# Kernel optimization log

Hardware: AMD Instinct MI355X
Metric: run time of the kernel (lower is better)

Reference implementation:

```python
import jax, jax.numpy as jnp
import numpy as np

E = 2048        # embed_dim
H = 16          # num_heads
HKV = 4         # num_heads_kv (GQA)
D = 128         # head_dim
DCONV = 4       # causal depthwise conv width
ROT_DIM = 128   # rotary_emb_dim (= head_dim, full rotation)
ROT_BASE = 10000.0
QKV_DIM = D * (H + 2 * HKV)  # 3072
B, S = 2, 2048


def setup_inputs() -> dict:
    key = jax.random.key(0)
    ks = jax.random.split(key, 7)
    return {
        "x": jax.random.normal(ks[0], (B, S, E), jnp.float32),
        "W_in": jax.random.normal(ks[1], (E, QKV_DIM), jnp.float32) * 0.02,
        "b_in": jax.random.normal(ks[2], (QKV_DIM,), jnp.float32) * 0.02,
        "conv_w": jax.random.normal(ks[3], (QKV_DIM, DCONV), jnp.float32) * 0.1,
        "conv_b": jax.random.normal(ks[4], (QKV_DIM,), jnp.float32) * 0.02,
        "W_out": jax.random.normal(ks[5], (E, E), jnp.float32) * 0.02,
        "b_out": jax.random.normal(ks[6], (E,), jnp.float32) * 0.02,
    }


def _rotary_cos_sin(seqlen, dtype):
    # flash_attn RotaryEmbedding: inv_freq over even indices
    inv_freq = 1.0 / (ROT_BASE ** (np.arange(0, ROT_DIM, 2, dtype=np.float32) / ROT_DIM))
    t = np.arange(seqlen, dtype=np.float32)
    freqs = np.outer(t, inv_freq)                      # [S, ROT_DIM/2]
    return jnp.asarray(np.cos(freqs), dtype), jnp.asarray(np.sin(freqs), dtype)


def _apply_rotary(xh, cos, sin):
    # non-interleaved: rotate halves of the first ROT_DIM dims. xh: [B,S,h,D]
    x1 = xh[..., : ROT_DIM // 2]
    x2 = xh[..., ROT_DIM // 2 : ROT_DIM]
    c = cos[None, :, None, :]
    s = sin[None, :, None, :]
    rot = jnp.concatenate([x1 * c - x2 * s, x2 * c + x1 * s], axis=-1)
    return jnp.concatenate([rot, xh[..., ROT_DIM:]], axis=-1)


def _forward(x, W_in, b_in, conv_w, conv_b, W_out, b_out):
    b, s, _ = x.shape
    qkv = x @ W_in + b_in                              # [B,S,QKV_DIM]

    # causal depthwise conv1d (kernel DCONV, left-pad DCONV-1, trim right)
    xp = jnp.pad(qkv, ((0, 0), (DCONV - 1, 0), (0, 0)))
    conv = conv_b
    for k in range(DCONV):
        conv = conv + xp[:, k : k + s, :] * conv_w[:, k]
    qkv = conv                                         # [B,S,QKV_DIM]

    q, kv = jnp.split(qkv, [H * D], axis=-1)
    q = q.reshape(b, s, H, D)
    kv = kv.reshape(b, s, 2, HKV, D)
    k, v = kv[:, :, 0], kv[:, :, 1]                    # [B,S,HKV,D]

    cos, sin = _rotary_cos_sin(s, x.dtype)
    q = _apply_rotary(q, cos, sin)
    k = _apply_rotary(k, cos, sin)

    # GQA: repeat kv heads
    rep = H // HKV
    k = jnp.repeat(k, rep, axis=2)                     # [B,S,H,D]
    v = jnp.repeat(v, rep, axis=2)

    scale = 1.0 / np.sqrt(D)
    scores = jnp.einsum("bqhd,bkhd->bhqk", q, k) * scale
    causal = jnp.tril(jnp.ones((s, s), bool))
    scores = jnp.where(causal[None, None], scores, jnp.finfo(scores.dtype).min)
    probs = jax.nn.softmax(scores, axis=-1)
    ctx = jnp.einsum("bhqk,bkhd->bqhd", probs, v)      # [B,S,H,D]

    return ctx.reshape(b, s, H * D) @ W_out + b_out    # [B,S,E]


def reference(x, W_in, b_in, conv_w, conv_b, W_out, b_out):
    return _forward(x, W_in, b_in, conv_w, conv_b, W_out, b_out)
```

## Files before the change

### kernel.cpp

```cpp
#include <hip/hip_runtime.h>
#include <hip/hip_bf16.h>

#define B_    2
#define S_    2048
#define E_    2048
#define H_    16
#define HKV_  4
#define D_    128
#define QKV_  3072

#define LOG2E  1.4426950408889634f
#define SCALE  0.08838834764831845f
#define SL     0.127517431f

typedef __attribute__((ext_vector_type(8))) short short8;
typedef __attribute__((ext_vector_type(4))) float floatx4;

typedef __attribute__((address_space(1))) const unsigned int gu32;
typedef __attribute__((address_space(3))) unsigned int lu32;

__device__ __forceinline__ void load_lds16(const unsigned short* g, unsigned short* l) {
    __builtin_amdgcn_global_load_lds((gu32*)g, (lu32*)l, 16, 0, 0);
}

__device__ __forceinline__ float b2f(unsigned short u) {
    union { unsigned int i; float f; } v; v.i = ((unsigned int)u) << 16; return v.f;
}
__device__ __forceinline__ unsigned short f2b(float f) {
    union { float f; unsigned int i; } v; v.f = f;
    unsigned int r = v.i + 0x7FFFu + ((v.i >> 16) & 1u);
    return (unsigned short)(r >> 16);
}
__device__ __forceinline__ unsigned int fbits(float f) {
    union { float f; unsigned int i; } v; v.f = f; return v.i;
}
__device__ __forceinline__ float bits2f(unsigned int i) {
    union { unsigned int i; float f; } v; v.i = i; return v.f;
}

template<int N> __device__ __forceinline__ void waitcnt_vm() {
    static_assert(N >= 0 && N <= 8, "vmcnt out of range");
    if constexpr (N == 0) asm volatile("s_waitcnt vmcnt(0)" ::: "memory");
    else if constexpr (N == 1) asm volatile("s_waitcnt vmcnt(1)" ::: "memory");
    else if constexpr (N == 2) asm volatile("s_waitcnt vmcnt(2)" ::: "memory");
    else if constexpr (N == 3) asm volatile("s_waitcnt vmcnt(3)" ::: "memory");
    else if constexpr (N == 4) asm volatile("s_waitcnt vmcnt(4)" ::: "memory");
    else if constexpr (N == 5) asm volatile("s_waitcnt vmcnt(5)" ::: "memory");
    else if constexpr (N == 6) asm volatile("s_waitcnt vmcnt(6)" ::: "memory");
    else if constexpr (N == 7) asm volatile("s_waitcnt vmcnt(7)" ::: "memory");
    else asm volatile("s_waitcnt vmcnt(8)" ::: "memory");
}

__global__ __launch_bounds__(256) void cvt_f32_bf16(
    const float* __restrict__ src, unsigned short* __restrict__ dst, int n)
{
    int i = (blockIdx.x * 256 + threadIdx.x) * 4;
    if (i + 3 < n) {
        float4 v = *(const float4*)&src[i];
        ushort4 o;
        o.x = f2b(v.x); o.y = f2b(v.y); o.z = f2b(v.z); o.w = f2b(v.w);
        *(ushort4*)&dst[i] = o;
    }
}

__global__ __launch_bounds__(256) void transpose_f32_bf16(
    const float* __restrict__ src, unsigned short* __restrict__ dst,
    int R, int C)
{
    __shared__ unsigned short tile[32][33];
    const int c0 = blockIdx.x * 32, r0 = blockIdx.y * 32;
    const int tx = threadIdx.x, ty = threadIdx.y;
    #pragma unroll
    for (int i = 0; i < 4; i++)
        tile[ty + 8 * i][tx] = f2b(src[(size_t)(r0 + ty + 8 * i) * C + c0 + tx]);
    __syncthreads();
    #pragma unroll
    for (int i = 0; i < 4; i++)
        dst[(size_t)(c0 + ty + 8 * i) * R + r0 + tx] = tile[tx][ty + 8 * i];
}

__global__ __launch_bounds__(256) void transpose_bf16(
    const unsigned short* __restrict__ src, unsigned short* __restrict__ dst,
    int R, int C)
{
    __shared__ unsigned short tile[32][33];
    const size_t boff = (size_t)blockIdx.z * R * C;
    src += boff; dst += boff;
    const int c0 = blockIdx.x * 32, r0 = blockIdx.y * 32;
    const int tx = threadIdx.x, ty = threadIdx.y;
    #pragma unroll
    for (int i = 0; i < 4; i++)
        tile[ty + 8 * i][tx] = src[(size_t)(r0 + ty + 8 * i) * C + c0 + tx];
    __syncthreads();
    #pragma unroll
    for (int i = 0; i < 4; i++)
        dst[(size_t)(c0 + ty + 8 * i) * R + r0 + tx] = tile[tx][ty + 8 * i];
}

template<int WR, int QR, int LX>
__device__ __forceinline__ void stage_unit8(
    const unsigned short* __restrict__ G, unsigned short* ls,
    int uu, int g0, int K, int k0, int wave, int lane)
{
    #pragma unroll
    for (int l = 0; l < LX; ++l) {
        const int c    = wave * LX + l;
        const int rr   = c / (QR / 8);
        const int row0 = rr * WR + uu * QR + (c % (QR / 8)) * 8;
        const int srow = row0 + (lane >> 3);
        const int sg   = (lane & 7) ^ (lane >> 3);
        load_lds16(&G[(size_t)(g0 + srow) * K + k0 + sg * 8], &ls[row0 * 64]);
    }
}

template<int BN, int WM, int WN, int OUTF32>
__global__ __launch_bounds__(512, 2) void gemm8(
    const unsigned short* __restrict__ A, const unsigned short* __restrict__ Bt,
    const float* __restrict__ bias, void* __restrict__ Cv,
    int M, int N, int K)
{
    constexpr int BM   = 256;
    constexpr int WMR  = BM / WM, WNR = BN / WN;
    constexpr int QMR  = WMR / 2, QNR = WNR / 2;
    constexpr int FM   = QMR / 16, FN = QNR / 16;
    constexpr int LA   = BM / 128, LB = BN / 128;
    constexpr int TILE = (BM + BN) * 64;

    __shared__ unsigned short lds[2 * TILE];

    const int tid  = threadIdx.x;
    const int wave = tid >> 6, lane = tid & 63;
    const int ln   = lane & 15, kq = lane >> 4;
    const int wm   = wave / WN, wn = wave % WN;

    const int nwg = gridDim.x;
    const int wg  = (blockIdx.x & 7) * (nwg >> 3) + (blockIdx.x >> 3);
    const int nbn = N / BN;
    const int m0  = (wg / nbn) * BM, n0 = (wg % nbn) * BN;

    floatx4 acc[2 * FM][2 * FN];
    #pragma unroll
    for (int i = 0; i < 2 * FM; ++i)
        #pragma unroll
        for (int j = 0; j < 2 * FN; ++j) {
            acc[i][j][0] = 0.f; acc[i][j][1] = 0.f;
            acc[i][j][2] = 0.f; acc[i][j][3] = 0.f;
        }

    stage_unit8<WMR, QMR, LA>(A,  &lds[0],       0, m0, K, 0, wave, lane);
    stage_unit8<WNR, QNR, LB>(Bt, &lds[BM * 64], 0, n0, K, 0, wave, lane);
    stage_unit8<WNR, QNR, LB>(Bt, &lds[BM * 64], 1, n0, K, 0, wave, lane);
    stage_unit8<WMR, QMR, LA>(A,  &lds[0],       1, m0, K, 0, wave, lane);
    waitcnt_vm<LA + LB>();
    __builtin_amdgcn_s_barrier();

    const int NT = K >> 6;
    int cur = 0;

    for (int t = 0; t < NT - 1; ++t) {
        const unsigned short* Asp = &lds[cur * TILE];
        const unsigned short* Bsp = Asp + BM * 64;
        unsigned short* Ssp = &lds[(cur ^ 1) * TILE];
        const int k1 = (t + 1) << 6;
        #pragma unroll
        for (int p = 0; p < 4; ++p) {
            const int qm = p >> 1, qn = p & 1;
            short8 af[2][FM], bg[2][FN];
            #pragma unroll
            for (int ks = 0; ks < 2; ++ks) {
                #pragma unroll
                for (int i = 0; i < FM; ++i)
                    af[ks][i] = *(const short8*)&Asp[(wm * WMR + qm * QMR + i * 16 + ln) * 64
                                                     + (((ks * 4 + kq) ^ (ln & 7)) * 8)];
                #pragma unroll
                for (int j = 0; j < FN; ++j)
                    bg[ks][j] = *(const short8*)&Bsp[(wn * WNR + qn * QNR + j * 16 + ln) * 64
                                                     + (((ks * 4 + kq) ^ (ln & 7)) * 8)];
            }
            if (p == 0)      stage_unit8<WMR, QMR, LA>(A,  Ssp,           0, m0, K, k1, wave, lane);
            else if (p == 1) stage_unit8<WNR, QNR, LB>(Bt, Ssp + BM * 64, 0, n0, K, k1, wave, lane);
            else if (p == 2) stage_unit8<WNR, QNR, LB>(Bt, Ssp + BM * 64, 1, n0, K, k1, wave, lane);
            else             stage_unit8<WMR, QMR, LA>(A,  Ssp,           1, m0, K, k1, wave, lane);
            __builtin_amdgcn_s_barrier();
            __builtin_amdgcn_s_setprio(1);
            #pragma unroll
            for (int ks = 0; ks < 2; ++ks)
                #pragma unroll
                for (int i = 0; i < FM; ++i)
                    #pragma unroll
                    for (int j = 0; j < FN; ++j)
                        acc[qm * FM + i][qn * FN + j] = __builtin_amdgcn_mfma_f32_16x16x32_bf16(
                            af[ks][i], bg[ks][j], acc[qm * FM + i][qn * FN + j], 0, 0, 0);
            __builtin_amdgcn_s_setprio(0);
            if (p == 0)      waitcnt_vm<2 * LA>();
            else if (p == 1) waitcnt_vm<LA + LB>();
            else if (p == 2) waitcnt_vm<LA + 2 * LB>();
            else             waitcnt_vm<LA + LB>();
            __builtin_amdgcn_s_barrier();
        }
        cur ^= 1;
    }

    asm volatile("s_waitcnt vmcnt(0)" ::: "memory");
    __builtin_amdgcn_s_barrier();
    {
        const unsigned short* Asp = &lds[cur * TILE];
        const unsigned short* Bsp = Asp + BM * 64;
        #pragma unroll
        for (int p = 0; p < 4; ++p) {
            const int qm = p >> 1, qn = p & 1;
            short8 af[2][FM], bg[2][FN];
            #pragma unroll
            for (int ks = 0; ks < 2; ++ks) {
                #pragma unroll
                for (int i = 0; i < FM; ++i)
                    af[ks][i] = *(const short8*)&Asp[(wm * WMR + qm * QMR + i * 16 + ln) * 64
                                                     + (((ks * 4 + kq) ^ (ln & 7)) * 8)];
                #pragma unroll
                for (int j = 0; j < FN; ++j)
                    bg[ks][j] = *(const short8*)&Bsp[(wn * WNR + qn * QNR + j * 16 + ln) * 64
                                                     + (((ks * 4 + kq) ^ (ln & 7)) * 8)];
            }
            __builtin_amdgcn_s_setprio(1);
            #pragma unroll
            for (int ks = 0; ks < 2; ++ks)
                #pragma unroll
                for (int i = 0; i < FM; ++i)
                    #pragma unroll
                    for (int j = 0; j < FN; ++j)
                        acc[qm * FM + i][qn * FN + j] = __builtin_amdgcn_mfma_f32_16x16x32_bf16(
                            af[ks][i], bg[ks][j], acc[qm * FM + i][qn * FN + j], 0, 0, 0);
            __builtin_amdgcn_s_setprio(0);
        }
    }

    #pragma unroll
    for (int nj = 0; nj < 2 * FN; ++nj) {
        const int col = n0 + wn * WNR + nj * 16 + ln;
        const float bv = bias[col];
        #pragma unroll
        for (int mi = 0; mi < 2 * FM; ++mi) {
            const int rowb = m0 + wm * WMR + mi * 16 + kq * 4;
            #pragma unroll
            for (int r = 0; r < 4; ++r) {
                const float val = acc[mi][nj][r] + bv;
                if (OUTF32) ((float*)Cv)[(size_t)(rowb + r) * N + col] = val;
                else ((unsigned short*)Cv)[(size_t)(rowb + r) * N + col] = f2b(val);
            }
        }
    }
}

__device__ __forceinline__ float conv_at(
    const unsigned short* __restrict__ qb, const float* __restrict__ cw,
    const float* __restrict__ cb, int s, int c)
{
    float acc = cb[c];
    const float* w = cw + c * 4;
    #pragma unroll
    for (int t = 0; t < 4; t++) {
        int sp = s - 3 + t;
        if (sp >= 0) acc += b2f(qb[(size_t)sp * QKV_ + c]) * w[t];
    }
    return acc;
}

__global__ __launch_bounds__(256) void conv_rot(
    const unsigned short* __restrict__ qkv, const float* __restrict__ cw,
    const float* __restrict__ cb, unsigned short* __restrict__ qo,
    unsigned short* __restrict__ ko, unsigned short* __restrict__ vo)
{
    const int bs = blockIdx.x;
    const int b = bs >> 11, s = bs & 2047;
    const unsigned short* qb = qkv + (size_t)b * S_ * QKV_;

    for (int it = threadIdx.x; it < 1792; it += 256) {
        if (it < 1280) {
            const int isq = it < 1024;
            const int rel = isq ? it : it - 1024;
            const int head = rel >> 6, d = rel & 63;
            const int c1 = (isq ? head * 128 : 2048 + head * 128) + d;
            float x1 = conv_at(qb, cw, cb, s, c1);
            float x2 = conv_at(qb, cw, cb, s, c1 + 64);
            float inv = exp2f((float)d * -0.2076205059304601f);
            float ang = (float)s * inv;
            float sn, cs;
            __sincosf(ang, &sn, &cs);
            float r1 = x1 * cs - x2 * sn;
            float r2 = x2 * cs + x1 * sn;
            unsigned short* dst = isq
                ? qo + ((size_t)(b * H_   + head) * S_ + s) * D_
                : ko + ((size_t)(b * HKV_ + head) * S_ + s) * D_;
            dst[d]      = f2b(r1);
            dst[d + 64] = f2b(r2);
        } else {
            const int idx = it - 1280;
            const int g = idx >> 7, d = idx & 127;
            float vv = conv_at(qb, cw, cb, s, 2560 + idx);
            vo[((size_t)(b * HKV_ + g) * S_ + s) * D_ + d] = f2b(vv);
        }
    }
}

__global__ __launch_bounds__(256, 4) void attn(
    const unsigned short* __restrict__ q, const unsigned short* __restrict__ k,
    const unsigned short* __restrict__ vT, unsigned short* __restrict__ ctx)
{
    __shared__ unsigned short Ks[64 * 128];
    __shared__ unsigned short Vs[128 * 64];
    __shared__ unsigned short Ps[4][16][64];

    const int h = blockIdx.x, qt = 31 - blockIdx.y, b = blockIdx.z, g = h >> 2;
    const int tid = threadIdx.x, wave = tid >> 6, lane = tid & 63;
    const int ln = lane & 15, kq = lane >> 4;

    const unsigned short* qh = q  + (size_t)(b * H_   + h) * S_ * D_;
    const unsigned short* kh = k  + (size_t)(b * HKV_ + g) * S_ * D_;
    const unsigned short* vh = vT + (size_t)(b * HKV_ + g) * D_ * S_;

    const int rK = (lane >> 4);
    const int pK = lane & 15;
    const int rV = (lane >> 3);
    const int pV = lane & 7;

    const int qrow0 = qt * 64 + wave * 16;

    short8 qf[4];
    #pragma unroll
    for (int f = 0; f < 4; f++)
        qf[f] = *(const short8*)&qh[(size_t)(qrow0 + ln) * D_ + f * 32 + kq * 8];

    floatx4 o[8];
    #pragma unroll
    for (int i = 0; i < 8; i++) { o[i][0] = 0.f; o[i][1] = 0.f; o[i][2] = 0.f; o[i][3] = 0.f; }
    float mr = -INFINITY, lr = 0.f;

    for (int kt = 0; kt <= qt; kt++) {
        __syncthreads();
        #pragma unroll
        for (int c = 0; c < 4; c++) {
            const int chunk = wave * 4 + c;
            int r  = chunk * 4 + rK;
            int gc = pK ^ (r & 15);
            load_lds16(&kh[(size_t)(kt * 64 + r) * D_ + gc * 8], &Ks[chunk * 512]);
            int rv = chunk * 8 + rV;
            int gv = pV ^ (rv & 7);
            load_lds16(&vh[(size_t)rv * S_ + kt * 64 + gv * 8], &Vs[chunk * 512]);
        }
        __syncthreads();

        floatx4 scv[4];
        #pragma unroll
        for (int nb = 0; nb < 4; nb++) { scv[nb][0]=0.f; scv[nb][1]=0.f; scv[nb][2]=0.f; scv[nb][3]=0.f; }
        #pragma unroll
        for (int ks = 0; ks < 4; ks++) {
            #pragma unroll
            for (int nb = 0; nb < 4; nb++) {
                short8 kf = *(const short8*)&Ks[(nb * 16 + ln) * 128 + (((ks * 4 + kq) ^ ln) * 8)];
                scv[nb] = __builtin_amdgcn_mfma_f32_16x16x32_bf16(kf, qf[ks], scv[nb], 0, 0, 0);
            }
        }

        if (kt == qt) {
            const int qloc = wave * 16 + ln;
            #pragma unroll
            for (int nb = 0; nb < 4; nb++)
                #pragma unroll
                for (int r = 0; r < 4; r++)
                    if (nb * 16 + kq * 4 + r > qloc) scv[nb][r] = -INFINITY;
        }

        float mx = -INFINITY;
        #pragma unroll
        for (int nb = 0; nb < 4; nb++) {
            float a0 = fmaxf(scv[nb][0], scv[nb][1]);
            float a1 = fmaxf(scv[nb][2], scv[nb][3]);
            mx = fmaxf(mx, fmaxf(a0, a1));
        }
        mx = fmaxf(mx, __shfl_xor(mx, 16));
        mx = fmaxf(mx, __shfl_xor(mx, 32));
        float mt = fmaxf(mr, mx);
        float al = exp2f((mr - mt) * SL);
        mr = mt;

        float rs = 0.f;
        #pragma unroll
        for (int nb = 0; nb < 4; nb++) {
            const int gct = 2 * nb + (kq >> 1);
            const int pbase = ((gct ^ (ln & 7)) << 3) + ((kq & 1) << 2);
            #pragma unroll
            for (int rr = 0; rr < 2; rr++) {
                unsigned int u0 = fbits(exp2f((scv[nb][2 * rr]     - mt) * SL));
                unsigned int u1 = fbits(exp2f((scv[nb][2 * rr + 1] - mt) * SL));
                rs += bits2f(u0 & 0xFFFF0000u) + bits2f(u1 & 0xFFFF0000u);
                *(unsigned int*)&Ps[wave][ln][pbase + 2 * rr] =
                    (u0 >> 16) | (u1 & 0xFFFF0000u);
            }
        }
        rs += __shfl_xor(rs, 16);
        rs += __shfl_xor(rs, 32);
        lr = lr * al + rs;

        float alr[4];
        #pragma unroll
        for (int r = 0; r < 4; r++) alr[r] = __shfl(al, kq * 4 + r);
        #pragma unroll
        for (int dn = 0; dn < 8; dn++)
            #pragma unroll
            for (int r = 0; r < 4; r++) o[dn][r] *= alr[r];

        short8 pa0 = *(const short8*)&Ps[wave][ln][(kq ^ (ln & 7)) << 3];
        short8 pa1 = *(const short8*)&Ps[wave][ln][((4 + kq) ^ (ln & 7)) << 3];
        #pragma unroll
        for (int dn = 0; dn < 8; dn++) {
            short8 b0 = *(const short8*)&Vs[(dn * 16 + ln) * 64 + ((kq ^ (ln & 7)) * 8)];
            o[dn] = __builtin_amdgcn_mfma_f32_16x16x32_bf16(pa0, b0, o[dn], 0, 0, 0);
            short8 b1 = *(const short8*)&Vs[(dn * 16 + ln) * 64 + (((4 + kq) ^ (ln & 7)) * 8)];
            o[dn] = __builtin_amdgcn_mfma_f32_16x16x32_bf16(pa1, b1, o[dn], 0, 0, 0);
        }
    }

    float lrr[4];
    #pragma unroll
    for (int r = 0; r < 4; r++) lrr[r] = 1.0f / __shfl(lr, kq * 4 + r);
    #pragma unroll
    for (int r = 0; r < 4; r++) {
        size_t rowoff = (size_t)(b * S_ + qt * 64 + wave * 16 + kq * 4 + r) * (H_ * D_) + h * D_;
        #pragma unroll
        for (int dn = 0; dn < 8; dn++)
            ctx[rowoff + dn * 16 + ln] = f2b(o[dn][r] * lrr[r]);
    }
}

extern "C" void kernel_launch(void* const* d_in, const int* in_sizes, int n_in,
                              void* d_out, int out_size, void* d_ws, size_t ws_size,
                              hipStream_t stream)
{
    const float* x     = (const float*)d_in[0];
    const float* W_in  = (const float*)d_in[1];
    const float* b_in  = (const float*)d_in[2];
    const float* cw    = (const float*)d_in[3];
    const float* cb    = (const float*)d_in[4];
    const float* W_out = (const float*)d_in[5];
    const float* b_out = (const float*)d_in[6];
    float* out = (float*)d_out;
    char* ws = (char*)d_ws;

    const size_t MB = 1024 * 1024;
    unsigned short* WtIn  = (unsigned short*)(ws);
    unsigned short* WtOut = (unsigned short*)(ws + 12 * MB);
    unsigned short* x16   = (unsigned short*)(ws + 20 * MB);
    unsigned short* qkv   = (unsigned short*)(ws + 36 * MB);
    unsigned short* qa    = (unsigned short*)(ws + 60 * MB);
    unsigned short* ka    = (unsigned short*)(ws + 76 * MB);
    unsigned short* va    = (unsigned short*)(ws + 80 * MB);
    unsigned short* vTa   = (unsigned short*)(ws + 84 * MB);
    unsigned short* ctx   = (unsigned short*)(ws + 20 * MB);

    dim3 tb(32, 8);
    hipLaunchKernelGGL(cvt_f32_bf16, dim3(8192), dim3(256), 0, stream, x, x16, 8388608);
    hipLaunchKernelGGL(transpose_f32_bf16, dim3(96, 64), tb, 0, stream, W_in,  WtIn,  2048, 3072);
    hipLaunchKernelGGL(transpose_f32_bf16, dim3(64, 64), tb, 0, stream, W_out, WtOut, 2048, 2048);
    hipLaunchKernelGGL((gemm8<256, 2, 4, 0>), dim3(192), dim3(512), 0, stream,
                       x16, WtIn, b_in, (void*)qkv, 4096, 3072, 2048);
    hipLaunchKernelGGL(conv_rot, dim3(4096), dim3(256), 0, stream, qkv, cw, cb, qa, ka, va);
    hipLaunchKernelGGL(transpose_bf16, dim3(4, 64, 8), tb, 0, stream, va, vTa, 2048, 128);
    hipLaunchKernelGGL(attn, dim3(16, 32, 2), dim3(256), 0, stream, qa, ka, vTa, ctx);
    hipLaunchKernelGGL((gemm8<128, 4, 2, 1>), dim3(256), dim3(512), 0, stream,
                       ctx, WtOut, b_out, (void*)out, 4096, 2048, 2048);
}
```

Baseline: 380.5 us.

## Register-prefetch next K/V tile, defer softmax rescale, raise MFMA priority

Replaces the direct global-to-LDS K/V loads with register prefetch of the next tile, issued right after the barrier so the global latency overlaps the current tile's MFMA work, followed by swizzled LDS stores. Adds a lazy online-softmax rescale that skips the output rescaling unless the running max grows beyond a threshold in some lane. Wraps the MFMA loops with s_setprio to favour matrix issue. The prefetch costs extra VGPRs, which may lower occupancy, and the deferred rescale lets unnormalized exponentials grow within the threshold bound.

```diff
diff --git a/kernel.cpp b/kernel.cpp
--- a/kernel.cpp
+++ b/kernel.cpp
@@ -12,6 +12,7 @@
 #define LOG2E  1.4426950408889634f
 #define SCALE  0.08838834764831845f
 #define SL     0.127517431f
+#define DEFER_THR 62.7f
 
 typedef __attribute__((ext_vector_type(8))) short short8;
 typedef __attribute__((ext_vector_type(4))) float floatx4;
@@ -335,23 +336,39 @@
     for (int i = 0; i < 8; i++) { o[i][0] = 0.f; o[i][1] = 0.f; o[i][2] = 0.f; o[i][3] = 0.f; }
     float mr = -INFINITY, lr = 0.f;
 
+    short8 kpre[4], vpre[4];
+    #pragma unroll
+    for (int c = 0; c < 4; c++) {
+        const int chunk = wave * 4 + c;
+        kpre[c] = *(const short8*)&kh[(size_t)(chunk * 4 + rK) * D_ + pK * 8];
+        vpre[c] = *(const short8*)&vh[(size_t)(chunk * 8 + rV) * S_ + pV * 8];
+    }
+
     for (int kt = 0; kt <= qt; kt++) {
         __syncthreads();
         #pragma unroll
         for (int c = 0; c < 4; c++) {
             const int chunk = wave * 4 + c;
-            int r  = chunk * 4 + rK;
-            int gc = pK ^ (r & 15);
-            load_lds16(&kh[(size_t)(kt * 64 + r) * D_ + gc * 8], &Ks[chunk * 512]);
-            int rv = chunk * 8 + rV;
-            int gv = pV ^ (rv & 7);
-            load_lds16(&vh[(size_t)rv * S_ + kt * 64 + gv * 8], &Vs[chunk * 512]);
+            const int r  = chunk * 4 + rK;
+            const int rv = chunk * 8 + rV;
+            *(short8*)&Ks[r * 128 + ((pK ^ (r & 15)) * 8)] = kpre[c];
+            *(short8*)&Vs[rv * 64 + ((pV ^ (rv & 7)) * 8)] = vpre[c];
         }
         __syncthreads();
 
+        if (kt < qt) {
+            #pragma unroll
+            for (int c = 0; c < 4; c++) {
+                const int chunk = wave * 4 + c;
+                kpre[c] = *(const short8*)&kh[(size_t)((kt + 1) * 64 + chunk * 4 + rK) * D_ + pK * 8];
+                vpre[c] = *(const short8*)&vh[(size_t)(chunk * 8 + rV) * S_ + (kt + 1) * 64 + pV * 8];
+            }
+        }
+
         floatx4 scv[4];
         #pragma unroll
         for (int nb = 0; nb < 4; nb++) { scv[nb][0]=0.f; scv[nb][1]=0.f; scv[nb][2]=0.f; scv[nb][3]=0.f; }
+        __builtin_amdgcn_s_setprio(1);
         #pragma unroll
         for (int ks = 0; ks < 4; ks++) {
             #pragma unroll
@@ -360,6 +377,7 @@
                 scv[nb] = __builtin_amdgcn_mfma_f32_16x16x32_bf16(kf, qf[ks], scv[nb], 0, 0, 0);
             }
         }
+        __builtin_amdgcn_s_setprio(0);
 
         if (kt == qt) {
             const int qloc = wave * 16 + ln;
@@ -379,9 +397,20 @@
         }
         mx = fmaxf(mx, __shfl_xor(mx, 16));
         mx = fmaxf(mx, __shfl_xor(mx, 32));
-        float mt = fmaxf(mr, mx);
-        float al = exp2f((mr - mt) * SL);
-        mr = mt;
+
+        float mt = mr, al = 1.0f;
+        if (!__all(mx - mr <= DEFER_THR)) {
+            mt = fmaxf(mr, mx);
+            al = exp2f((mr - mt) * SL);
+            mr = mt;
+            float alr[4];
+            #pragma unroll
+            for (int r = 0; r < 4; r++) alr[r] = __shfl(al, kq * 4 + r);
+            #pragma unroll
+            for (int dn = 0; dn < 8; dn++)
+                #pragma unroll
+                for (int r = 0; r < 4; r++) o[dn][r] *= alr[r];
+        }
 
         float rs = 0.f;
         #pragma unroll
@@ -401,16 +430,9 @@
         rs += __shfl_xor(rs, 32);
         lr = lr * al + rs;
 
-        float alr[4];
-        #pragma unroll
-        for (int r = 0; r < 4; r++) alr[r] = __shfl(al, kq * 4 + r);
-        #pragma unroll
-        for (int dn = 0; dn < 8; dn++)
-            #pragma unroll
-            for (int r = 0; r < 4; r++) o[dn][r] *= alr[r];
-
         short8 pa0 = *(const short8*)&Ps[wave][ln][(kq ^ (ln & 7)) << 3];
         short8 pa1 = *(const short8*)&Ps[wave][ln][((4 + kq) ^ (ln & 7)) << 3];
+        __builtin_amdgcn_s_setprio(1);
         #pragma unroll
         for (int dn = 0; dn < 8; dn++) {
             short8 b0 = *(const short8*)&Vs[(dn * 16 + ln) * 64 + ((kq ^ (ln & 7)) * 8)];
@@ -418,6 +440,7 @@
             short8 b1 = *(const short8*)&Vs[(dn * 16 + ln) * 64 + (((4 + kq) ^ (ln & 7)) * 8)];
             o[dn] = __builtin_amdgcn_mfma_f32_16x16x32_bf16(pa1, b1, o[dn], 0, 0, 0);
         }
+        __builtin_amdgcn_s_setprio(0);
     }
 
     float lrr[4];
```

Result: slower. 444.8 us (+16.9%).
